# Kernel optimization log

Hardware: AMD Instinct MI355X
Metric: run time of the kernel (lower is better)

The kernel has to match this reference:

```python
import jax, jax.numpy as jnp
import numpy as np
from jax import lax


def _gru_pass(x_proj, h0, w_hh, b_hh):
    # Faithful to torch: unbatched GRU scanning sequentially over the n_sample axis
    # with a single shared hidden state. x_proj: (N, 3H) = x @ w_ih.T + b_ih.
    def cell(h, xp):
        gh = jnp.dot(w_hh, h) + b_hh              # (3H,)
        xr, xz, xn = jnp.split(xp, 3)
        hr, hz, hn = jnp.split(gh, 3)
        r = jax.nn.sigmoid(xr + hr)
        z = jax.nn.sigmoid(xz + hz)
        n = jnp.tanh(xn + r * hn)
        h_new = (1.0 - z) * n + z * h
        return h_new, h_new
    h_last, outs = lax.scan(cell, h0, x_proj)
    return outs, h_last                            # (N, H), (H,)


def setup_inputs() -> dict:
    key = jax.random.key(0)
    ks = jax.random.split(key, 6)
    H = 50
    s = 0.2  # ~ torch default init scale for these fan-ins
    return {
        "w_ih": jax.random.normal(ks[0], (3 * H, 2), jnp.float32) * s,
        "w_hh": jax.random.normal(ks[1], (3 * H, H), jnp.float32) * s,
        "b_ih": jax.random.normal(ks[2], (3 * H,), jnp.float32) * s,
        "b_hh": jax.random.normal(ks[3], (3 * H,), jnp.float32) * s,
        "fc_w": jax.random.normal(ks[4], (2, H), jnp.float32) * s,
        "fc_b": jax.random.normal(ks[5], (2,), jnp.float32) * s,
        "sorb": 64,
        "n_sample": 4096,
    }


def reference(w_ih, w_hh, b_ih, b_hh, fc_w, fc_b, sorb, n_sample):
    H = w_hh.shape[1]
    baseline = float(sorb // 2 - 1)
    base_key = jax.random.key(42)
    x0 = jnp.zeros((n_sample, 2), jnp.float32)     # samples[:, 0, :] == 0
    h0 = jnp.zeros((H,), jnp.float32)
    nup0 = jnp.zeros((n_sample,), jnp.float32)

    def heaviside(x):
        # 0.5*(sign(sign(x)+0.1)+1): 1 for x >= 0, else 0
        return (x >= 0.0).astype(jnp.float32)

    def step(carry, i):
        x, h, num_up = carry
        x_proj = x @ w_ih.T + b_ih                 # (N, 3H)
        outs, h_new = _gru_pass(x_proj, h, w_hh, b_hh)
        logits = outs @ fc_w.T + fc_b              # (N, 2)
        out = jnp.sqrt(jax.nn.softmax(logits, axis=1))  # sqsoftmax
        # occupation-number masking, active for i >= sorb/2
        num_down = i.astype(jnp.float32) - num_up
        act_up = heaviside(baseline - num_up)
        act_down = heaviside(baseline - num_down)
        masked = out * jnp.stack([act_down, act_up], axis=1)
        masked = masked / jnp.clip(
            jnp.linalg.norm(masked, axis=1, keepdims=True), 1e-30, None)
        out = jnp.where(i >= sorb / 2, masked, out)
        # multinomial over 2 classes (weights need not sum to 1)
        p0 = out[:, 0] / jnp.clip(out[:, 0] + out[:, 1], 1e-30, None)
        u = jax.random.uniform(jax.random.fold_in(base_key, i), (n_sample,))
        s = (u >= p0).astype(jnp.int32)            # 1 == class 1 ("up")
        x_next = jax.nn.one_hot(s, 2, dtype=jnp.float32)
        return (x_next, h_new, num_up + s.astype(jnp.float32)), s

    _, samples = lax.scan(step, (x0, h0, nup0), jnp.arange(sorb))
    # torch returns argmax over the one-hot == sampled class index
    return samples.T                                # (n_sample, sorb) int32
```

## Files before the change

### kernel.cpp

```cpp
#include <hip/hip_runtime.h>
#include <cstdint>

#pragma clang fp contract(off)

#define RNG_VARIANT 0
#define GEMV_VARIANT 0
#define LOGIT_VARIANT 0

#define HH 50
#define H3 150
#define SORB 64
#define NSAMP 4096
#define TOT (SORB * NSAMP)

__device__ __forceinline__ float xla_tanh(float x) {
  const float kClamp = 7.90531110763549805f;
  float ax = fabsf(x);
  float xc = fminf(fmaxf(x, -kClamp), kClamp);
  float x2 = xc * xc;
  float p = -2.76076847742355e-16f;
  p = x2 * p + 2.00018790482477e-13f;
  p = x2 * p + -8.60467152213735e-11f;
  p = x2 * p + 5.12229709037114e-08f;
  p = x2 * p + 1.48572235717979e-05f;
  p = x2 * p + 6.37261928875436e-04f;
  p = x2 * p + 4.89352455891786e-03f;
  p = xc * p;
  float q = 1.19825839466702e-06f;
  q = x2 * q + 1.18534705686654e-04f;
  q = x2 * q + 2.26843463243900e-03f;
  q = x2 * q + 4.89352518554385e-03f;
  float r = p / q;
  return (ax < 0.0004f) ? x : r;
}

__device__ __forceinline__ float xla_logistic(float x) {
  return 0.5f + 0.5f * xla_tanh(x * 0.5f);
}

__device__ __forceinline__ float exp_cr(float x) {
  return (float)exp((double)x);
}

__device__ __forceinline__ void tf2x32(uint32_t k0, uint32_t k1,
                                       uint32_t c0, uint32_t c1,
                                       uint32_t& o0, uint32_t& o1) {
  uint32_t k2 = k0 ^ k1 ^ 0x1BD11BDAu;
  uint32_t x0 = c0 + k0, x1 = c1 + k1;
#define TF_R(d) { x0 += x1; x1 = (x1 << (d)) | (x1 >> (32 - (d))); x1 ^= x0; }
#define TF_GA TF_R(13) TF_R(15) TF_R(26) TF_R(6)
#define TF_GB TF_R(17) TF_R(29) TF_R(16) TF_R(24)
  TF_GA; x0 += k1; x1 += k2 + 1u;
  TF_GB; x0 += k2; x1 += k0 + 2u;
  TF_GA; x0 += k0; x1 += k1 + 3u;
  TF_GB; x0 += k1; x1 += k2 + 4u;
  TF_GA; x0 += k2; x1 += k0 + 5u;
#undef TF_GB
#undef TF_GA
#undef TF_R
  o0 = x0; o1 = x1;
}

__device__ __forceinline__ float u_for_cell(int cc) {
  int ii = cc >> 12;
  int jj = cc & (NSAMP - 1);
  uint32_t k0, k1;
  tf2x32(0u, 42u, 0u, (uint32_t)ii, k0, k1);
  uint32_t b0, b1, bits;
#if RNG_VARIANT == 0
  tf2x32(k0, k1, 0u, (uint32_t)jj, b0, b1);
  bits = b0 ^ b1;
#elif RNG_VARIANT == 1
  tf2x32(k0, k1, 0u, (uint32_t)jj, b0, b1);
  bits = b0;
#else
  if (jj < NSAMP / 2) { tf2x32(k0, k1, (uint32_t)jj, (uint32_t)(jj + NSAMP / 2), b0, b1); bits = b0; }
  else                { tf2x32(k0, k1, (uint32_t)(jj - NSAMP / 2), (uint32_t)jj, b0, b1); bits = b1; }
#endif
  return __uint_as_float((bits >> 9) | 0x3f800000u) - 1.0f;
}

extern "C" __global__ void __launch_bounds__(256, 1)
ARSampler_59244778881183_kernel(const float* __restrict__ w_ih,
                                const float* __restrict__ w_hh,
                                const float* __restrict__ b_ih,
                                const float* __restrict__ b_hh,
                                const float* __restrict__ fc_w,
                                const float* __restrict__ fc_b,
                                int* __restrict__ out) {
  __shared__ float sh_h[64];
  __shared__ float sh_gh[160];
  __shared__ float sh_xp[3][160];
  __shared__ float sh_fcw[2][56];
  __shared__ float sh_fcb[2];
  __shared__ float sh_outs[32][56];
  __shared__ float sh_u[2][16];
  __shared__ float sh_nu[NSAMP];
  __shared__ unsigned char sh_bits[2][NSAMP];

  const int t = threadIdx.x;

  for (int idx = t; idx < H3; idx += 256) {
    float b = b_ih[idx];
    sh_xp[0][idx] = w_ih[idx * 2 + 0] + b;
    sh_xp[1][idx] = w_ih[idx * 2 + 1] + b;
    sh_xp[2][idx] = b;
  }
  for (int idx = t; idx < 2 * HH; idx += 256) sh_fcw[idx / HH][idx % HH] = fc_w[idx];
  if (t < 2) sh_fcb[t] = fc_b[t];
  if (t < HH) sh_h[t] = 0.0f;
  for (int idx = t; idx < NSAMP; idx += 256) sh_nu[idx] = 0.0f;

  float wreg[HH];
  float bhh = 0.0f;
  if (t < H3) {
#pragma unroll
    for (int k = 0; k < HH; ++k) wreg[k] = w_hh[t * HH + k];
    bhh = b_hh[t];
  }
  __syncthreads();

  auto do_sample = [&](int cbase, int ts) {
    int cc = cbase + ts;
    int ii = cc >> 12;
    int jj = cc & (NSAMP - 1);
    const float* o = sh_outs[cc & 31];
    float l0, l1;
#if LOGIT_VARIANT == 0
    l0 = 0.0f; l1 = 0.0f;
#pragma unroll
    for (int k = 0; k < HH; ++k) {
      l0 = fmaf(o[k], sh_fcw[0][k], l0);
      l1 = fmaf(o[k], sh_fcw[1][k], l1);
    }
#else
    l0 = o[0] * sh_fcw[0][0]; l1 = o[0] * sh_fcw[1][0];
#pragma unroll
    for (int k = 1; k < HH; ++k) {
      l0 = l0 + o[k] * sh_fcw[0][k];
      l1 = l1 + o[k] * sh_fcw[1][k];
    }
#endif
    l0 = l0 + sh_fcb[0];
    l1 = l1 + sh_fcb[1];
    float mx = fmaxf(l0, l1);
    float e0 = exp_cr(l0 - mx);
    float e1 = exp_cr(l1 - mx);
    float se = e0 + e1;
    float o0 = sqrtf(e0 / se);
    float o1 = sqrtf(e1 / se);
    float nuo = sh_nu[jj];
    if (ii >= SORB / 2) {
      float fi = (float)ii;
      float ndown = fi - nuo;
      float ad = ((31.0f - ndown) >= 0.0f) ? 1.0f : 0.0f;
      float au = ((31.0f - nuo) >= 0.0f) ? 1.0f : 0.0f;
      float m0 = o0 * ad;
      float m1 = o1 * au;
      float nr = sqrtf(m0 * m0 + m1 * m1);
      nr = fmaxf(nr, 1e-30f);
      o0 = m0 / nr;
      o1 = m1 / nr;
    }
    float den = fmaxf(o0 + o1, 1e-30f);
    float p0 = o0 / den;
    float u = sh_u[(cbase >> 4) & 1][ts];
    int s = (u >= p0) ? 1 : 0;
    sh_nu[jj] = nuo + (float)s;
    sh_bits[ii & 1][jj] = (unsigned char)s;
    out[jj * SORB + ii] = s;
  };

  for (int c = 0; c < TOT; ++c) {
    const int i = c >> 12;
    const int j = c & (NSAMP - 1);

    if (t < H3) {
      float hv[HH];
#pragma unroll
      for (int k = 0; k < HH; ++k) hv[k] = sh_h[k];
#if GEMV_VARIANT == 0
      float acc[8];
#pragma unroll
      for (int l = 0; l < 8; ++l) acc[l] = wreg[l] * hv[l];
#pragma unroll
      for (int ch = 1; ch < 6; ++ch) {
#pragma unroll
        for (int l = 0; l < 8; ++l) acc[l] = acc[l] + wreg[8 * ch + l] * hv[8 * ch + l];
      }
      float s04 = acc[0] + acc[4];
      float s15 = acc[1] + acc[5];
      float s26 = acc[2] + acc[6];
      float s37 = acc[3] + acc[7];
      float t0 = s04 + s26;
      float t1 = s15 + s37;
      float dot = t0 + t1;
      dot = dot + wreg[48] * hv[48];
      dot = dot + wreg[49] * hv[49];
#else
      float dot = wreg[0] * hv[0];
#pragma unroll
      for (int k = 1; k < HH; ++k) dot = dot + wreg[k] * hv[k];
#endif
      sh_gh[t] = dot + bhh;
    } else if ((c & 15) == 0) {
      if (t >= 192 && t < 208) {
        if (c > 0) do_sample(c - 16, t - 192);
      } else if (t >= 208 && t < 224) {
        sh_u[(c >> 4) & 1][t - 208] = u_for_cell(c + (t - 208));
      }
    }
    __syncthreads();

    if (t < HH) {
      int sel = (i == 0) ? 2 : (int)sh_bits[(i - 1) & 1][j];
      float xr = sh_xp[sel][t];
      float xz = sh_xp[sel][t + 50];
      float xn = sh_xp[sel][t + 100];
      float hr = sh_gh[t];
      float hz = sh_gh[t + 50];
      float hn = sh_gh[t + 100];
      float r = xla_logistic(xr + hr);
      float z = xla_logistic(xz + hz);
      float rhn = r * hn;
      float n = xla_tanh(xn + rhn);
      float hold = sh_h[t];
      float omz = 1.0f - z;
      float hnew = omz * n + z * hold;
      sh_h[t] = hnew;
      sh_outs[j & 31][t] = hnew;
    }
    __syncthreads();
  }

  if (t >= 192 && t < 208) do_sample(TOT - 16, t - 192);
}

extern "C" void kernel_launch(void* const* d_in, const int* in_sizes, int n_in,
                              void* d_out, int out_size, void* d_ws, size_t ws_size,
                              hipStream_t stream) {
  (void)in_sizes; (void)n_in; (void)out_size; (void)d_ws; (void)ws_size;
  const float* w_ih = (const float*)d_in[0];
  const float* w_hh = (const float*)d_in[1];
  const float* b_ih = (const float*)d_in[2];
  const float* b_hh = (const float*)d_in[3];
  const float* fc_w = (const float*)d_in[4];
  const float* fc_b = (const float*)d_in[5];
  hipLaunchKernelGGL(ARSampler_59244778881183_kernel, dim3(1), dim3(256), 0, stream,
                     w_ih, w_hh, b_ih, b_hh, fc_w, fc_b, (int*)d_out);
}
```

Before: 183.2 ms.

## Run GRU recurrence in one wavefront with barrier-free ring handoff to sampler wave

The 150-thread GEMV plus two __syncthreads per step is replaced by a single 64-lane wavefront. Each lane computes all three gate rows for its hidden unit from registers, so no block barrier is needed per step. Hidden states go into a 128-slot shared ring with a sequence tag, and a second wavefront spins on that tag to do the logits, softmax, masking and sampling for 64 cells at a time. This removes the per-step barrier latency, at the cost of spin-wait flags with a fuel limit and memory-ordering assumptions between wavefronts.

```diff
diff --git a/kernel.cpp b/kernel.cpp
--- a/kernel.cpp
+++ b/kernel.cpp
@@ -3,15 +3,16 @@
 
 #pragma clang fp contract(off)
 
-#define RNG_VARIANT 0
-#define GEMV_VARIANT 0
-#define LOGIT_VARIANT 0
-
 #define HH 50
-#define H3 150
 #define SORB 64
 #define NSAMP 4096
 #define TOT (SORB * NSAMP)
+#define RSLOTS 128
+#define RSTRIDE 56
+#define SPIN_FUEL (1 << 16)
+
+typedef __attribute__((ext_vector_type(2))) float v2f;
+typedef __attribute__((ext_vector_type(4))) float v4f;
 
 __device__ __forceinline__ float xla_tanh(float x) {
   const float kClamp = 7.90531110763549805f;
@@ -66,21 +67,35 @@
   int jj = cc & (NSAMP - 1);
   uint32_t k0, k1;
   tf2x32(0u, 42u, 0u, (uint32_t)ii, k0, k1);
-  uint32_t b0, b1, bits;
-#if RNG_VARIANT == 0
+  uint32_t b0, b1;
   tf2x32(k0, k1, 0u, (uint32_t)jj, b0, b1);
-  bits = b0 ^ b1;
-#elif RNG_VARIANT == 1
-  tf2x32(k0, k1, 0u, (uint32_t)jj, b0, b1);
-  bits = b0;
-#else
-  if (jj < NSAMP / 2) { tf2x32(k0, k1, (uint32_t)jj, (uint32_t)(jj + NSAMP / 2), b0, b1); bits = b0; }
-  else                { tf2x32(k0, k1, (uint32_t)(jj - NSAMP / 2), (uint32_t)jj, b0, b1); bits = b1; }
-#endif
+  uint32_t bits = b0 ^ b1;
   return __uint_as_float((bits >> 9) | 0x3f800000u) - 1.0f;
 }
 
-extern "C" __global__ void __launch_bounds__(256, 1)
+__device__ __forceinline__ float dot_xla(const v2f* __restrict__ w,
+                                         const v2f* __restrict__ h) {
+  v2f A0 = w[0] * h[0];
+  v2f A1 = w[1] * h[1];
+  v2f A2 = w[2] * h[2];
+  v2f A3 = w[3] * h[3];
+#pragma unroll
+  for (int ch = 1; ch < 6; ++ch) {
+    A0 = A0 + w[4 * ch + 0] * h[4 * ch + 0];
+    A1 = A1 + w[4 * ch + 1] * h[4 * ch + 1];
+    A2 = A2 + w[4 * ch + 2] * h[4 * ch + 2];
+    A3 = A3 + w[4 * ch + 3] * h[4 * ch + 3];
+  }
+  v2f S0 = A0 + A2;
+  v2f S1 = A1 + A3;
+  v2f T = S0 + S1;
+  float dot = T.x + T.y;
+  dot = dot + w[24].x * h[24].x;
+  dot = dot + w[24].y * h[24].y;
+  return dot;
+}
+
+extern "C" __global__ void __launch_bounds__(128, 1)
 ARSampler_59244778881183_kernel(const float* __restrict__ w_ih,
                                 const float* __restrict__ w_hh,
                                 const float* __restrict__ b_ih,
@@ -88,152 +103,167 @@
                                 const float* __restrict__ fc_w,
                                 const float* __restrict__ fc_b,
                                 int* __restrict__ out) {
-  __shared__ float sh_h[64];
-  __shared__ float sh_gh[160];
-  __shared__ float sh_xp[3][160];
-  __shared__ float sh_fcw[2][56];
-  __shared__ float sh_fcb[2];
-  __shared__ float sh_outs[32][56];
-  __shared__ float sh_u[2][16];
+  __shared__ __align__(16) float ring[RSLOTS][RSTRIDE];
   __shared__ float sh_nu[NSAMP];
   __shared__ unsigned char sh_bits[2][NSAMP];
+  __shared__ unsigned int sh_done;
 
   const int t = threadIdx.x;
-
-  for (int idx = t; idx < H3; idx += 256) {
-    float b = b_ih[idx];
-    sh_xp[0][idx] = w_ih[idx * 2 + 0] + b;
-    sh_xp[1][idx] = w_ih[idx * 2 + 1] + b;
-    sh_xp[2][idx] = b;
-  }
-  for (int idx = t; idx < 2 * HH; idx += 256) sh_fcw[idx / HH][idx % HH] = fc_w[idx];
-  if (t < 2) sh_fcb[t] = fc_b[t];
-  if (t < HH) sh_h[t] = 0.0f;
-  for (int idx = t; idx < NSAMP; idx += 256) sh_nu[idx] = 0.0f;
-
-  float wreg[HH];
-  float bhh = 0.0f;
-  if (t < H3) {
-#pragma unroll
-    for (int k = 0; k < HH; ++k) wreg[k] = w_hh[t * HH + k];
-    bhh = b_hh[t];
+  const int lane = t & 63;
+
+  if (t < 64) {
+    for (int s = lane; s < RSLOTS; s += 64)
+      ring[s][HH] = __uint_as_float(~0u);
+    if (lane < HH) ring[RSLOTS - 1][lane] = 0.0f;
+  } else {
+    if (lane == 0) sh_done = 0u;
+    for (int q = lane; q < NSAMP; q += 64) sh_nu[q] = 0.0f;
   }
   __syncthreads();
 
-  auto do_sample = [&](int cbase, int ts) {
-    int cc = cbase + ts;
-    int ii = cc >> 12;
-    int jj = cc & (NSAMP - 1);
-    const float* o = sh_outs[cc & 31];
-    float l0, l1;
-#if LOGIT_VARIANT == 0
-    l0 = 0.0f; l1 = 0.0f;
+  if (t < 64) {
+    const int tr = (lane < HH) ? lane : 0;
+
+    v2f wA[25], wB[25], wC[25];
+#pragma unroll
+    for (int k = 0; k < 25; ++k) {
+      wA[k] = v2f{w_hh[tr * HH + 2 * k], w_hh[tr * HH + 2 * k + 1]};
+      wB[k] = v2f{w_hh[(tr + 50) * HH + 2 * k], w_hh[(tr + 50) * HH + 2 * k + 1]};
+      wC[k] = v2f{w_hh[(tr + 100) * HH + 2 * k], w_hh[(tr + 100) * HH + 2 * k + 1]};
+    }
+    const float bhr = b_hh[tr], bhz = b_hh[tr + 50], bhn = b_hh[tr + 100];
+    const float xrb = b_ih[tr], xzb = b_ih[tr + 50], xnb = b_ih[tr + 100];
+    const float xr0 = w_ih[tr * 2 + 0] + xrb;
+    const float xr1 = w_ih[tr * 2 + 1] + xrb;
+    const float xz0 = w_ih[(tr + 50) * 2 + 0] + xzb;
+    const float xz1 = w_ih[(tr + 50) * 2 + 1] + xzb;
+    const float xn0 = w_ih[(tr + 100) * 2 + 0] + xnb;
+    const float xn1 = w_ih[(tr + 100) * 2 + 1] + xnb;
+    float hold = 0.0f;
+
+    volatile unsigned int* donep = &sh_done;
+
+    for (int c = 0; c < TOT; ++c) {
+      const int i = c >> 12;
+      const int j = c & (NSAMP - 1);
+
+      if ((c & 63) == 0 && c >= RSLOTS) {
+        int fuel = SPIN_FUEL;
+        while (*donep < (unsigned)(c - 64) && --fuel)
+          __builtin_amdgcn_s_sleep(2);
+        asm volatile("" ::: "memory");
+      }
+
+      const float* rp = ring[(c + RSLOTS - 1) & (RSLOTS - 1)];
+      v2f hv[25];
+#pragma unroll
+      for (int m = 0; m < 13; ++m) {
+        v4f f = *(const v4f*)(rp + 4 * m);
+        hv[2 * m] = v2f{f.x, f.y};
+        if (2 * m + 1 < 25) hv[2 * m + 1] = v2f{f.z, f.w};
+      }
+
+      float xr, xz, xn;
+      if (i == 0) {
+        xr = xrb; xz = xzb; xn = xnb;
+      } else {
+        unsigned b = sh_bits[(i - 1) & 1][j];
+        xr = b ? xr1 : xr0;
+        xz = b ? xz1 : xz0;
+        xn = b ? xn1 : xn0;
+      }
+
+      const float ghr = dot_xla(wA, hv) + bhr;
+      const float ghz = dot_xla(wB, hv) + bhz;
+      const float ghn = dot_xla(wC, hv) + bhn;
+
+      const float r = xla_logistic(xr + ghr);
+      const float z = xla_logistic(xz + ghz);
+      const float rhn = r * ghn;
+      const float n = xla_tanh(xn + rhn);
+      const float omz = 1.0f - z;
+      const float hnew = omz * n + z * hold;
+      hold = hnew;
+
+      const int wi = (lane < HH) ? lane : HH;
+      const float wd = (lane < HH) ? hnew : __uint_as_float((unsigned)c);
+      ring[c & (RSLOTS - 1)][wi] = wd;
+    }
+  } else {
+    float fw0[HH], fw1[HH];
 #pragma unroll
     for (int k = 0; k < HH; ++k) {
-      l0 = fmaf(o[k], sh_fcw[0][k], l0);
-      l1 = fmaf(o[k], sh_fcw[1][k], l1);
-    }
-#else
-    l0 = o[0] * sh_fcw[0][0]; l1 = o[0] * sh_fcw[1][0];
-#pragma unroll
-    for (int k = 1; k < HH; ++k) {
-      l0 = l0 + o[k] * sh_fcw[0][k];
-      l1 = l1 + o[k] * sh_fcw[1][k];
-    }
-#endif
-    l0 = l0 + sh_fcb[0];
-    l1 = l1 + sh_fcb[1];
-    float mx = fmaxf(l0, l1);
-    float e0 = exp_cr(l0 - mx);
-    float e1 = exp_cr(l1 - mx);
-    float se = e0 + e1;
-    float o0 = sqrtf(e0 / se);
-    float o1 = sqrtf(e1 / se);
-    float nuo = sh_nu[jj];
-    if (ii >= SORB / 2) {
-      float fi = (float)ii;
-      float ndown = fi - nuo;
-      float ad = ((31.0f - ndown) >= 0.0f) ? 1.0f : 0.0f;
-      float au = ((31.0f - nuo) >= 0.0f) ? 1.0f : 0.0f;
-      float m0 = o0 * ad;
-      float m1 = o1 * au;
-      float nr = sqrtf(m0 * m0 + m1 * m1);
-      nr = fmaxf(nr, 1e-30f);
-      o0 = m0 / nr;
-      o1 = m1 / nr;
-    }
-    float den = fmaxf(o0 + o1, 1e-30f);
-    float p0 = o0 / den;
-    float u = sh_u[(cbase >> 4) & 1][ts];
-    int s = (u >= p0) ? 1 : 0;
-    sh_nu[jj] = nuo + (float)s;
-    sh_bits[ii & 1][jj] = (unsigned char)s;
-    out[jj * SORB + ii] = s;
-  };
-
-  for (int c = 0; c < TOT; ++c) {
-    const int i = c >> 12;
-    const int j = c & (NSAMP - 1);
-
-    if (t < H3) {
-      float hv[HH];
-#pragma unroll
-      for (int k = 0; k < HH; ++k) hv[k] = sh_h[k];
-#if GEMV_VARIANT == 0
-      float acc[8];
-#pragma unroll
-      for (int l = 0; l < 8; ++l) acc[l] = wreg[l] * hv[l];
-#pragma unroll
-      for (int ch = 1; ch < 6; ++ch) {
-#pragma unroll
-        for (int l = 0; l < 8; ++l) acc[l] = acc[l] + wreg[8 * ch + l] * hv[8 * ch + l];
-      }
-      float s04 = acc[0] + acc[4];
-      float s15 = acc[1] + acc[5];
-      float s26 = acc[2] + acc[6];
-      float s37 = acc[3] + acc[7];
-      float t0 = s04 + s26;
-      float t1 = s15 + s37;
-      float dot = t0 + t1;
-      dot = dot + wreg[48] * hv[48];
-      dot = dot + wreg[49] * hv[49];
-#else
-      float dot = wreg[0] * hv[0];
-#pragma unroll
-      for (int k = 1; k < HH; ++k) dot = dot + wreg[k] * hv[k];
-#endif
-      sh_gh[t] = dot + bhh;
-    } else if ((c & 15) == 0) {
-      if (t >= 192 && t < 208) {
-        if (c > 0) do_sample(c - 16, t - 192);
-      } else if (t >= 208 && t < 224) {
-        sh_u[(c >> 4) & 1][t - 208] = u_for_cell(c + (t - 208));
-      }
-    }
-    __syncthreads();
-
-    if (t < HH) {
-      int sel = (i == 0) ? 2 : (int)sh_bits[(i - 1) & 1][j];
-      float xr = sh_xp[sel][t];
-      float xz = sh_xp[sel][t + 50];
-      float xn = sh_xp[sel][t + 100];
-      float hr = sh_gh[t];
-      float hz = sh_gh[t + 50];
-      float hn = sh_gh[t + 100];
-      float r = xla_logistic(xr + hr);
-      float z = xla_logistic(xz + hz);
-      float rhn = r * hn;
-      float n = xla_tanh(xn + rhn);
-      float hold = sh_h[t];
-      float omz = 1.0f - z;
-      float hnew = omz * n + z * hold;
-      sh_h[t] = hnew;
-      sh_outs[j & 31][t] = hnew;
-    }
-    __syncthreads();
+      fw0[k] = fc_w[k];
+      fw1[k] = fc_w[HH + k];
+    }
+    const float fb0 = fc_b[0], fb1 = fc_b[1];
+
+    for (int B = 0; B < TOT; B += 64) {
+      const int cc = B + lane;
+      const int ii = B >> 12;
+      const int jj = cc & (NSAMP - 1);
+
+      {
+        const unsigned target = (unsigned)(B + 63);
+        volatile unsigned int* sp =
+            (volatile unsigned int*)&ring[(B + 63) & (RSLOTS - 1)][HH];
+        int fuel = SPIN_FUEL;
+        while (*sp != target && --fuel) __builtin_amdgcn_s_sleep(2);
+        __builtin_amdgcn_s_sleep(1);
+        asm volatile("s_waitcnt lgkmcnt(0)" ::: "memory");
+      }
+
+      const float* op = ring[cc & (RSLOTS - 1)];
+      float o[52];
+#pragma unroll
+      for (int m = 0; m < 13; ++m) {
+        v4f f = *(const v4f*)(op + 4 * m);
+        o[4 * m + 0] = f.x; o[4 * m + 1] = f.y;
+        o[4 * m + 2] = f.z; o[4 * m + 3] = f.w;
+      }
+
+      float l0 = 0.0f, l1 = 0.0f;
+#pragma unroll
+      for (int k = 0; k < HH; ++k) {
+        l0 = fmaf(o[k], fw0[k], l0);
+        l1 = fmaf(o[k], fw1[k], l1);
+      }
+      l0 = l0 + fb0;
+      l1 = l1 + fb1;
+
+      const float mx = fmaxf(l0, l1);
+      const float e0 = exp_cr(l0 - mx);
+      const float e1 = exp_cr(l1 - mx);
+      const float se = e0 + e1;
+      float o0 = sqrtf(e0 / se);
+      float o1 = sqrtf(e1 / se);
+
+      const float nuo = sh_nu[jj];
+      if (ii >= SORB / 2) {
+        const float fi = (float)ii;
+        const float ndown = fi - nuo;
+        const float ad = ((31.0f - ndown) >= 0.0f) ? 1.0f : 0.0f;
+        const float au = ((31.0f - nuo) >= 0.0f) ? 1.0f : 0.0f;
+        const float m0 = o0 * ad;
+        const float m1 = o1 * au;
+        float nr = sqrtf(m0 * m0 + m1 * m1);
+        nr = fmaxf(nr, 1e-30f);
+        o0 = m0 / nr;
+        o1 = m1 / nr;
+      }
+      const float den = fmaxf(o0 + o1, 1e-30f);
+      const float p0 = o0 / den;
+      const float u = u_for_cell(cc);
+      const int s = (u >= p0) ? 1 : 0;
+
+      sh_nu[jj] = nuo + (float)s;
+      sh_bits[ii & 1][jj] = (unsigned char)s;
+      out[jj * SORB + ii] = s;
+
+      asm volatile("" ::: "memory");
+      *(volatile unsigned int*)&sh_done = (unsigned)(B + 64);
+    }
   }
-
-  if (t >= 192 && t < 208) do_sample(TOT - 16, t - 192);
 }
 
 extern "C" void kernel_launch(void* const* d_in, const int* in_sizes, int n_in,
@@ -246,6 +276,6 @@
   const float* b_hh = (const float*)d_in[3];
   const float* fc_w = (const float*)d_in[4];
   const float* fc_b = (const float*)d_in[5];
-  hipLaunchKernelGGL(ARSampler_59244778881183_kernel, dim3(1), dim3(256), 0, stream,
+  hipLaunchKernelGGL(ARSampler_59244778881183_kernel, dim3(1), dim3(128), 0, stream,
                      w_ih, w_hh, b_ih, b_hh, fc_w, fc_b, (int*)d_out);
 }
```

New measurement: 169.6 ms. -7.4%, faster.
